# Optimization experiments

Measured on AMD Instinct MI355X. Metric: run time of the kernel, lower is better.

Reference implementation:

```python
import jax, jax.numpy as jnp
import numpy as np

ROPE_THETA = 10000.0

def _apply_rope(t):
    # t: [B, H, S, D]; rotate interleaved even/odd pairs
    B, H, S, D = t.shape
    inv_freq = 1.0 / (ROPE_THETA ** (jnp.arange(0, D, 2, dtype=jnp.float32) / D))  # [D/2]
    ang = jnp.arange(S, dtype=jnp.float32)[:, None] * inv_freq[None, :]            # [S, D/2]
    cos = jnp.cos(ang)[None, None]  # [1,1,S,D/2]
    sin = jnp.sin(ang)[None, None]
    te = t[..., 0::2]
    to = t[..., 1::2]
    re = te * cos - to * sin
    ro = te * sin + to * cos
    out = jnp.stack([re, ro], axis=-1).reshape(B, H, S, D)
    return out

def setup_inputs() -> dict:
    key = jax.random.key(0)
    ks = jax.random.split(key, 5)
    B, S, DIM = 2, 2048, 2048
    x = jax.random.normal(ks[0], (B, S, DIM), dtype=jnp.float32)
    scale = 0.02
    Wq = jax.random.normal(ks[1], (DIM, DIM), dtype=jnp.float32) * scale
    Wk = jax.random.normal(ks[2], (DIM, DIM), dtype=jnp.float32) * scale
    Wv = jax.random.normal(ks[3], (DIM, DIM), dtype=jnp.float32) * scale
    Wo = jax.random.normal(ks[4], (DIM, DIM), dtype=jnp.float32) * scale
    return {"x": x, "Wq": Wq, "Wk": Wk, "Wv": Wv, "Wo": Wo}

def reference(x, Wq, Wk, Wv, Wo):
    B, S, DIM = x.shape
    H = 16
    HD = DIM // H
    # nn.Linear(bias=False) with weight [out,in]: y = x @ W.T; here W stored [in,out]
    q = (x @ Wq).reshape(B, S, H, HD).transpose(0, 2, 1, 3)  # [B,H,S,HD]
    k = (x @ Wk).reshape(B, S, H, HD).transpose(0, 2, 1, 3)
    v = (x @ Wv).reshape(B, S, H, HD).transpose(0, 2, 1, 3)
    q = _apply_rope(q)
    k = _apply_rope(k)
    scores = jnp.einsum('bhqd,bhkd->bhqk', q, k) / jnp.sqrt(jnp.float32(HD))  # [B,H,S,S]
    causal = jnp.tril(jnp.ones((S, S), dtype=bool))
    scores = jnp.where(causal[None, None], scores, jnp.float32(-jnp.inf))
    attn = jax.nn.softmax(scores, axis=-1)
    out = jnp.einsum('bhqk,bhkd->bhqd', attn, v)            # [B,H,S,HD]
    out = out.transpose(0, 2, 1, 3).reshape(B, S, DIM)
    return out @ Wo  # output projection (dropout is identity in eval)
```

## Files before the change

### kernel.cpp

```cpp
#include <hip/hip_runtime.h>
#include <hip/hip_bf16.h>
#include <math.h>

typedef __bf16 bf16;
typedef __attribute__((ext_vector_type(2))) __bf16 bf16x2;
typedef __attribute__((ext_vector_type(4))) __bf16 bf16x4;
typedef __attribute__((ext_vector_type(8))) __bf16 bf16x8;
typedef __attribute__((ext_vector_type(4))) float f32x4;

#define LDS_ASYNC16(gptr, lptr)                                                        \
  __builtin_amdgcn_global_load_lds(                                                    \
      (const __attribute__((address_space(1))) void*)(gptr),                           \
      (__attribute__((address_space(3))) void*)(lptr), 16, 0, 0)

constexpr int BATCH = 2, SEQ = 2048, DIM = 2048, NH = 16, HD = 128;
constexpr float QSC = 0.12751744f;
constexpr float FREQC = 0.20762050593046f;

template <int CTRL>
__device__ __forceinline__ float dpp_mov_f(float x) {
  return __int_as_float(__builtin_amdgcn_update_dpp(
      __float_as_int(x), __float_as_int(x), CTRL, 0xf, 0xf, false));
}
__device__ __forceinline__ float rowmax16(float x) {
  x = fmaxf(x, dpp_mov_f<0x121>(x));
  x = fmaxf(x, dpp_mov_f<0x122>(x));
  x = fmaxf(x, dpp_mov_f<0x124>(x));
  x = fmaxf(x, dpp_mov_f<0x128>(x));
  return x;
}
__device__ __forceinline__ float rowsum16(float x) {
  x += dpp_mov_f<0x121>(x);
  x += dpp_mov_f<0x122>(x);
  x += dpp_mov_f<0x124>(x);
  x += dpp_mov_f<0x128>(x);
  return x;
}

__global__ void cvt_f32_to_bf16(const float4* __restrict__ in,
                                bf16x4* __restrict__ out, int n4) {
  int i = blockIdx.x * blockDim.x + threadIdx.x;
  if (i >= n4) return;
  float4 v = in[i];
  bf16x4 o;
  o[0] = (bf16)v.x; o[1] = (bf16)v.y; o[2] = (bf16)v.z; o[3] = (bf16)v.w;
  out[i] = o;
}

__global__ void transpose_w4(const float* __restrict__ W0, const float* __restrict__ W1,
                             const float* __restrict__ W2, const float* __restrict__ W3,
                             bf16* __restrict__ T0, bf16* __restrict__ T3) {
  __shared__ float tile[32][33];
  const int z = blockIdx.z;
  const float* W = (z == 0) ? W0 : (z == 1) ? W1 : (z == 2) ? W2 : W3;
  bf16* WT = (z == 3) ? T3 : (T0 + (size_t)z * DIM * DIM);
  int tx = threadIdx.x, ty = threadIdx.y;
  int bx = blockIdx.x * 32, by = blockIdx.y * 32;
#pragma unroll
  for (int j = 0; j < 32; j += 8)
    tile[ty + j][tx] = W[(size_t)(by + ty + j) * DIM + bx + tx];
  __syncthreads();
#pragma unroll
  for (int j = 0; j < 32; j += 8)
    WT[(size_t)(bx + ty + j) * DIM + by + tx] = (bf16)tile[tx][ty + j];
}


__global__ __launch_bounds__(256) void gemm_qkv(const bf16* __restrict__ A,
                                                const bf16* __restrict__ BT,
                                                bf16* __restrict__ Qb,
                                                bf16* __restrict__ Kb,
                                                bf16* __restrict__ VTo) {
  __shared__ __attribute__((aligned(16))) bf16 As[128 * 64];
  __shared__ __attribute__((aligned(16))) bf16 Bs[128 * 64];
  const int tid = threadIdx.x;
  const int w = tid >> 6, lane = tid & 63;
  const int quad = lane >> 4, ln = lane & 15;
  const int m0 = blockIdx.y * 128, n0 = blockIdx.x * 128;
  const int wm = (w >> 1) * 64, wn = (w & 1) * 64;
  const int l7 = ln & 7;
  f32x4 acc[4][4] = {};

  for (int k0 = 0; k0 < DIM; k0 += 64) {
#pragma unroll
    for (int i = 0; i < 4; ++i) {
      const int c = i * 256 + tid;
      const int row = c >> 3, p = c & 7;
      LDS_ASYNC16(A  + (size_t)(m0 + row) * DIM + k0 + ((p ^ (row & 7)) * 8),
                  As + (size_t)(i * 256 + w * 64) * 8);
      LDS_ASYNC16(BT + (size_t)(n0 + row) * DIM + k0 + ((p ^ (row & 7)) * 8),
                  Bs + (size_t)(i * 256 + w * 64) * 8);
    }
    __syncthreads();
#pragma unroll
    for (int kh = 0; kh < 2; ++kh) {
      bf16x8 af[4], bfr[4];
#pragma unroll
      for (int t = 0; t < 4; ++t)
        af[t] = *(const bf16x8*)(As + (wm + t * 16 + ln) * 64 +
                                 (((kh * 4 + quad) ^ l7) * 8));
#pragma unroll
      for (int t = 0; t < 4; ++t)
        bfr[t] = *(const bf16x8*)(Bs + (wn + t * 16 + ln) * 64 +
                                  (((kh * 4 + quad) ^ l7) * 8));
#pragma unroll
      for (int mt = 0; mt < 4; ++mt)
#pragma unroll
        for (int nt = 0; nt < 4; ++nt)
          acc[mt][nt] = __builtin_amdgcn_mfma_f32_16x16x32_bf16(
              af[mt], bfr[nt], acc[mt][nt], 0, 0, 0);
    }
    __syncthreads();
  }

  const int sel = n0 >> 11;
  if (sel == 2) {
#pragma unroll
    for (int mt = 0; mt < 4; ++mt)
#pragma unroll
      for (int nt = 0; nt < 4; ++nt) {
        int gr = m0 + wm + mt * 16 + quad * 4;
        int fc = (n0 + wn + nt * 16 + ln) & 2047;
        int b = gr >> 11, s0 = gr & (SEQ - 1);
        int h = fc >> 7, d = fc & (HD - 1);
        bf16x4 pk;
#pragma unroll
        for (int r = 0; r < 4; ++r) pk[r] = (bf16)acc[mt][nt][r];
        *(bf16x4*)(VTo + ((size_t)((b * NH + h) * HD + d)) * SEQ + s0) = pk;
      }
  } else {
    bf16* Dst = sel ? Kb : Qb;
    const float osc = sel ? 1.0f : QSC;
#pragma unroll
    for (int nt = 0; nt < 4; ++nt) {
      int gc = n0 + wn + nt * 16 + ln;
      int fc = gc & 2047, d = fc & (HD - 1);
      float freq = exp2f(-(float)(d >> 1) * FREQC);
      bool ev = !(d & 1);
#pragma unroll
      for (int mt = 0; mt < 4; ++mt) {
#pragma unroll
        for (int r = 0; r < 4; ++r) {
          int gr = m0 + wm + mt * 16 + quad * 4 + r;
          int s = gr & (SEQ - 1);
          float ang = (float)s * freq;
          float sn, cs;
          __sincosf(ang, &sn, &cs);
          float own = acc[mt][nt][r];
          float oth = __shfl_xor(own, 1);
          float res = ev ? (own * cs - oth * sn) : (oth * sn + own * cs);
          Dst[(size_t)gr * DIM + fc] = (bf16)(res * osc);
        }
      }
    }
  }
}

template <int MODE>
__global__ __launch_bounds__(256) void gemm_bt(const bf16* __restrict__ A,
                                               const bf16* __restrict__ BT,
                                               void* __restrict__ C) {
  __shared__ __attribute__((aligned(16))) bf16 As[128 * 64];
  __shared__ __attribute__((aligned(16))) bf16 Bs[128 * 64];
  const int tid = threadIdx.x;
  const int w = tid >> 6, lane = tid & 63;
  const int quad = lane >> 4, ln = lane & 15;
  const int m0 = blockIdx.y * 128, n0 = blockIdx.x * 128;
  const int wm = (w >> 1) * 64, wn = (w & 1) * 64;
  const int l7 = ln & 7;
  f32x4 acc[4][4] = {};

  for (int k0 = 0; k0 < DIM; k0 += 64) {
#pragma unroll
    for (int i = 0; i < 4; ++i) {
      const int c = i * 256 + tid;
      const int row = c >> 3, p = c & 7;
      LDS_ASYNC16(A  + (size_t)(m0 + row) * DIM + k0 + ((p ^ (row & 7)) * 8),
                  As + (size_t)(i * 256 + w * 64) * 8);
      LDS_ASYNC16(BT + (size_t)(n0 + row) * DIM + k0 + ((p ^ (row & 7)) * 8),
                  Bs + (size_t)(i * 256 + w * 64) * 8);
    }
    __syncthreads();
#pragma unroll
    for (int kh = 0; kh < 2; ++kh) {
      bf16x8 af[4], bfr[4];
#pragma unroll
      for (int t = 0; t < 4; ++t)
        af[t] = *(const bf16x8*)(As + (wm + t * 16 + ln) * 64 +
                                 (((kh * 4 + quad) ^ l7) * 8));
#pragma unroll
      for (int t = 0; t < 4; ++t)
        bfr[t] = *(const bf16x8*)(Bs + (wn + t * 16 + ln) * 64 +
                                  (((kh * 4 + quad) ^ l7) * 8));
#pragma unroll
      for (int mt = 0; mt < 4; ++mt)
#pragma unroll
        for (int nt = 0; nt < 4; ++nt)
          acc[mt][nt] = __builtin_amdgcn_mfma_f32_16x16x32_bf16(
              af[mt], bfr[nt], acc[mt][nt], 0, 0, 0);
    }
    __syncthreads();
  }

  if (MODE == 0) {
    bf16* Co = (bf16*)C;
#pragma unroll
    for (int mt = 0; mt < 4; ++mt)
#pragma unroll
      for (int nt = 0; nt < 4; ++nt) {
        int gr = m0 + wm + mt * 16 + quad * 4;
        int gc = n0 + wn + nt * 16 + ln;
#pragma unroll
        for (int r = 0; r < 4; ++r)
          Co[(size_t)(gr + r) * DIM + gc] = (bf16)acc[mt][nt][r];
      }
  } else {
    float* Co = (float*)C;
#pragma unroll
    for (int mt = 0; mt < 4; ++mt)
#pragma unroll
      for (int nt = 0; nt < 4; ++nt) {
        int gr = m0 + wm + mt * 16 + quad * 4;
        int gc = n0 + wn + nt * 16 + ln;
#pragma unroll
        for (int r = 0; r < 4; ++r)
          Co[(size_t)(gr + r) * DIM + gc] = acc[mt][nt][r];
      }
  }
}

__device__ __forceinline__ int ml_off(int t) {
  return (t < 10) ? 2 * (t - 5) : (t < 15) ? 10 + 3 * (t - 10) : 25;
}
__device__ __forceinline__ int op_off(int t) {
  return (t < 10) ? (t - 5) : (t < 15) ? 5 + 2 * (t - 10) : 15;
}

constexpr int PSTR = 72;
__global__ __launch_bounds__(256) void flash_attn(
    const bf16* __restrict__ Q, const bf16* __restrict__ K,
    const bf16* __restrict__ VT, bf16* __restrict__ O,
    bf16* __restrict__ Opart, float* __restrict__ Mpart,
    float* __restrict__ Lpart) {
  __shared__ __attribute__((aligned(16))) bf16 Ks[64 * 128];
  __shared__ __attribute__((aligned(16))) bf16 VTs[128 * 64];
  __shared__ __attribute__((aligned(16))) bf16 Ps[4][32 * PSTR];
  const int tid = threadIdx.x;
  const int w = tid >> 6, lane = tid & 63, quad = lane >> 4, ln = lane & 15;
  const int lb = blockIdx.x;
  const int low3 = lb & 7, rest = lb >> 3;
  const int e = rest % 34;
  const int bh = (rest / 34) * 8 + low3;
  int t, c0, nc;
  if (e < 5)       { t = e;                  c0 = 0;               nc = 1; }
  else if (e < 15) { t = 5 + ((e - 5) >> 1); c0 = (e - 5) & 1;     nc = 2; }
  else if (e < 30) { int q = (e - 15) / 3;   t = 10 + q; c0 = (e - 15) - 3 * q; nc = 3; }
  else             { t = 15;                 c0 = e - 30;          nc = 4; }
  const int q0 = t * 128;
  const int ktN = 2 * (t + 1);
  const int kt0 = c0 * 10;
  const int kt1 = min(kt0 + 10, ktN);
  const bool chunked = (nc > 1);
  const int b = bh >> 4, h = bh & 15;

  bf16x8 qf[2][4];
#pragma unroll
  for (int mt = 0; mt < 2; ++mt)
#pragma unroll
    for (int kc = 0; kc < 4; ++kc)
      qf[mt][kc] = *(const bf16x8*)(Q + ((size_t)b * SEQ + q0 + w * 32 + mt * 16 + ln) * DIM +
                                    h * HD + kc * 32 + quad * 8);
  f32x4 o[2][8] = {};
  float mst[2][4], lst[2][4];
#pragma unroll
  for (int mt = 0; mt < 2; ++mt)
#pragma unroll
    for (int r = 0; r < 4; ++r) { mst[mt][r] = -1e30f; lst[mt][r] = 0.f; }

  for (int kt = kt0; kt < kt1; ++kt) {
    __syncthreads();
#pragma unroll
    for (int i = 0; i < 4; ++i) {
      const int c = i * 256 + tid;
      LDS_ASYNC16(K + ((size_t)b * SEQ + kt * 64 + (c >> 4)) * DIM + h * HD +
                      (((c & 15) ^ ((c >> 4) & 15)) * 8),
                  Ks + (size_t)(i * 256 + w * 64) * 8);
      LDS_ASYNC16(VT + ((size_t)((b * NH + h) * HD) + (c >> 3)) * SEQ + kt * 64 +
                      (((c & 7) ^ ((c >> 3) & 7)) * 8),
                  VTs + (size_t)(i * 256 + w * 64) * 8);
    }
    __syncthreads();

    f32x4 s[2][4] = {};
#pragma unroll
    for (int nt = 0; nt < 4; ++nt) {
      bf16x8 kf[4];
#pragma unroll
      for (int kc = 0; kc < 4; ++kc)
        kf[kc] = *(const bf16x8*)(Ks + (nt * 16 + ln) * 128 +
                                  (((kc * 4 + quad) ^ ln) * 8));
#pragma unroll
      for (int kc = 0; kc < 4; ++kc)
#pragma unroll
        for (int mt = 0; mt < 2; ++mt)
          s[mt][nt] = __builtin_amdgcn_mfma_f32_16x16x32_bf16(
              qf[mt][kc], kf[kc], s[mt][nt], 0, 0, 0);
    }

    const bool diag = (kt * 64 + 63 > q0);
    if (diag) {
#pragma unroll
      for (int mt = 0; mt < 2; ++mt)
#pragma unroll
        for (int nt = 0; nt < 4; ++nt)
#pragma unroll
          for (int r = 0; r < 4; ++r) {
            int kg = kt * 64 + nt * 16 + ln;
            int qg = q0 + w * 32 + mt * 16 + quad * 4 + r;
            if (kg > qg) s[mt][nt][r] = -1e30f;
          }
    }

#pragma unroll
    for (int mt = 0; mt < 2; ++mt)
#pragma unroll
      for (int r = 0; r < 4; ++r) {
        float rm = fmaxf(fmaxf(s[mt][0][r], s[mt][1][r]),
                         fmaxf(s[mt][2][r], s[mt][3][r]));
        rm = rowmax16(rm);
        float mold = mst[mt][r];
        float mnew = fmaxf(mold, rm);
        float alpha = exp2f(mold - mnew);
        mst[mt][r] = mnew;
        float rs = 0.f;
#pragma unroll
        for (int nt = 0; nt < 4; ++nt) {
          float p = exp2f(s[mt][nt][r] - mnew);
          rs += p;
          Ps[w][(mt * 16 + quad * 4 + r) * PSTR + nt * 16 + ln] = (bf16)p;
        }
        lst[mt][r] = lst[mt][r] * alpha + rs;
#pragma unroll
        for (int nd = 0; nd < 8; ++nd) o[mt][nd][r] *= alpha;
      }
    __syncthreads();

#pragma unroll
    for (int kc2 = 0; kc2 < 2; ++kc2) {
      bf16x8 pf[2];
#pragma unroll
      for (int mt = 0; mt < 2; ++mt)
        pf[mt] = *(const bf16x8*)(&Ps[w][(mt * 16 + ln) * PSTR + kc2 * 32 + quad * 8]);
#pragma unroll
      for (int nd = 0; nd < 8; ++nd) {
        bf16x8 vf = *(const bf16x8*)(VTs + (nd * 16 + ln) * 64 +
                                     (((kc2 * 4 + quad) ^ (ln & 7)) * 8));
#pragma unroll
        for (int mt = 0; mt < 2; ++mt)
          o[mt][nd] = __builtin_amdgcn_mfma_f32_16x16x32_bf16(
              pf[mt], vf, o[mt][nd], 0, 0, 0);
      }
    }
  }

  if (!chunked) {
#pragma unroll
    for (int mt = 0; mt < 2; ++mt)
#pragma unroll
      for (int r = 0; r < 4; ++r) {
        float inv = 1.f / rowsum16(lst[mt][r]);
        int qg = q0 + w * 32 + mt * 16 + quad * 4 + r;
#pragma unroll
        for (int nd = 0; nd < 8; ++nd)
          O[((size_t)b * SEQ + qg) * DIM + h * HD + nd * 16 + ln] =
              (bf16)(o[mt][nd][r] * inv);
      }
  } else {
    const int mls = bh * 29 + ml_off(t) + c0;
    bf16* Op = (c0 == 0) ? nullptr
                         : Opart + (size_t)(bh * 18 + op_off(t) + (c0 - 1)) * (128 * 128);
#pragma unroll
    for (int mt = 0; mt < 2; ++mt)
#pragma unroll
      for (int r = 0; r < 4; ++r) {
        float l = rowsum16(lst[mt][r]);
        int qr = w * 32 + mt * 16 + quad * 4 + r;
        if (ln == 0) {
          Mpart[mls * 128 + qr] = mst[mt][r];
          Lpart[mls * 128 + qr] = l;
        }
        if (c0 == 0) {
#pragma unroll
          for (int nd = 0; nd < 8; ++nd)
            O[((size_t)b * SEQ + q0 + qr) * DIM + h * HD + nd * 16 + ln] =
                (bf16)o[mt][nd][r];
        } else {
#pragma unroll
          for (int nd = 0; nd < 8; ++nd)
            Op[qr * 128 + nd * 16 + ln] = (bf16)o[mt][nd][r];
        }
      }
  }
}

__global__ __launch_bounds__(256) void flash_merge(const bf16* __restrict__ Opart,
                                                   const float* __restrict__ Mpart,
                                                   const float* __restrict__ Lpart,
                                                   bf16* __restrict__ O) {
  const int bh = blockIdx.x;
  const int t = 5 + blockIdx.y;
  const int nc = (t < 10) ? 2 : (t < 15) ? 3 : 4;
  const int b = bh >> 4, h = bh & 15;
  const int row = threadIdx.x >> 1, half = threadIdx.x & 1;
  const int mlb = bh * 29 + ml_off(t);
  float m[4], l[4], wt[4];
  float M = -1e30f;
  for (int c = 0; c < nc; ++c) {
    m[c] = Mpart[(mlb + c) * 128 + row];
    l[c] = Lpart[(mlb + c) * 128 + row];
    M = fmaxf(M, m[c]);
  }
  float wsum = 0.f;
  for (int c = 0; c < nc; ++c) { wt[c] = exp2f(m[c] - M); wsum += wt[c] * l[c]; }
  const float inv = 1.f / wsum;
  bf16* dst = O + ((size_t)b * SEQ + t * 128 + row) * DIM + h * HD + half * 64;
  const bf16* pb = Opart + (size_t)(bh * 18 + op_off(t)) * (128 * 128) + row * 128 + half * 64;
#pragma unroll
  for (int j = 0; j < 8; ++j) {
    bf16x8 a0 = *(const bf16x8*)(dst + j * 8);
    float acc[8];
#pragma unroll
    for (int k = 0; k < 8; ++k) acc[k] = wt[0] * (float)a0[k];
    for (int c = 1; c < nc; ++c) {
      bf16x8 a = *(const bf16x8*)(pb + (size_t)(c - 1) * (128 * 128) + j * 8);
#pragma unroll
      for (int k = 0; k < 8; ++k) acc[k] += wt[c] * (float)a[k];
    }
    bf16x8 o8;
#pragma unroll
    for (int k = 0; k < 8; ++k) o8[k] = (bf16)(acc[k] * inv);
    *(bf16x8*)(dst + j * 8) = o8;
  }
}

extern "C" void kernel_launch(void* const* d_in, const int* in_sizes, int n_in,
                              void* d_out, int out_size, void* d_ws, size_t ws_size,
                              hipStream_t stream) {
  (void)in_sizes; (void)n_in; (void)out_size; (void)ws_size;
  const float* x  = (const float*)d_in[0];
  const float* Wq = (const float*)d_in[1];
  const float* Wk = (const float*)d_in[2];
  const float* Wv = (const float*)d_in[3];
  const float* Wo = (const float*)d_in[4];

  char* ws = (char*)d_ws;
  const size_t MB = 1u << 20;
  const size_t WB = (size_t)DIM * DIM * 2;
  bf16* WTqkv = (bf16*)(ws);
  bf16* WoT   = (bf16*)(ws + 3 * WB);
  bf16* xb    = (bf16*)(ws + 32 * MB);
  bf16* Qb    = (bf16*)(ws + 48 * MB);
  bf16* Kb    = (bf16*)(ws + 64 * MB);
  bf16* VT    = (bf16*)(ws + 80 * MB);
  bf16* Ab    = xb;
  bf16*  Opart = (bf16*)(ws);
  float* Mpart = (float*)(ws + 19 * MB);
  float* Lpart = (float*)(ws + 19 * MB + 512 * 1024);

  int n4 = BATCH * SEQ * DIM / 4;
  cvt_f32_to_bf16<<<n4 / 256, 256, 0, stream>>>((const float4*)x, (bf16x4*)xb, n4);
  dim3 tb(32, 8), tg(DIM / 32, DIM / 32, 4);
  transpose_w4<<<tg, tb, 0, stream>>>(Wq, Wk, Wv, Wo, WTqkv, WoT);

  dim3 qg(3 * DIM / 128, BATCH * SEQ / 128);
  gemm_qkv<<<qg, 256, 0, stream>>>(xb, WTqkv, Qb, Kb, VT);

  flash_attn<<<34 * BATCH * NH, 256, 0, stream>>>(Qb, Kb, VT, Ab, Opart, Mpart, Lpart);
  dim3 mg(BATCH * NH, 11);
  flash_merge<<<mg, 256, 0, stream>>>(Opart, Mpart, Lpart, Ab);

  dim3 gg(DIM / 128, BATCH * SEQ / 128);
  gemm_bt<2><<<gg, 256, 0, stream>>>(Ab, WoT, d_out);
}
```

Before: 444.5 us.

## Rewrite QKV GEMM as 256x256 tile with multi-buffered async LDS pipeline

The fused QKV projection GEMM moves from a 128x128 tile with 4 waves and a single LDS buffer to a 256x256 tile with 8 waves. It now double-buffers K-slices in LDS, issuing async global-to-LDS loads for future slices while MFMAs run on the current one, and uses s_setprio around the MFMA bursts. A remapped 1D grid with block-id swizzling is added for L2 locality. The aim is to hide global-load latency and raise arithmetic intensity, at the cost of more registers per thread, more LDS and fewer workgroups (384).

```diff
diff --git a/kernel.cpp b/kernel.cpp
--- a/kernel.cpp
+++ b/kernel.cpp
@@ -65,88 +65,171 @@
     WT[(size_t)(bx + ty + j) * DIM + by + tx] = (bf16)tile[tx][ty + j];
 }
 
-
-__global__ __launch_bounds__(256) void gemm_qkv(const bf16* __restrict__ A,
+__device__ __forceinline__ void stage_half(const bf16* __restrict__ src, int g0, int ks,
+                                           bf16* lds, int w, int lane) {
+#pragma unroll
+  for (int j = 0; j < 2; ++j) {
+    const int u = (j * 8 + w) * 64 + lane;
+    const int row = u >> 2;
+    const int kc = (u & 3) ^ ((u >> 3) & 3);
+    LDS_ASYNC16(src + (size_t)(g0 + row) * DIM + ks + kc * 8,
+                lds + (size_t)((j * 8 + w) * 64) * 8);
+  }
+}
+
+__global__ __launch_bounds__(512) void gemm_qkv(const bf16* __restrict__ A,
                                                 const bf16* __restrict__ BT,
                                                 bf16* __restrict__ Qb,
                                                 bf16* __restrict__ Kb,
                                                 bf16* __restrict__ VTo) {
-  __shared__ __attribute__((aligned(16))) bf16 As[128 * 64];
-  __shared__ __attribute__((aligned(16))) bf16 Bs[128 * 64];
+  constexpr int RSZ = 256 * 32;
+  constexpr int NT = DIM / 64;
+  __shared__ __attribute__((aligned(16))) bf16 As[4 * RSZ];
+  __shared__ __attribute__((aligned(16))) bf16 Bs[4 * RSZ];
   const int tid = threadIdx.x;
   const int w = tid >> 6, lane = tid & 63;
   const int quad = lane >> 4, ln = lane & 15;
-  const int m0 = blockIdx.y * 128, n0 = blockIdx.x * 128;
-  const int wm = (w >> 1) * 64, wn = (w & 1) * 64;
-  const int l7 = ln & 7;
-  f32x4 acc[4][4] = {};
-
-  for (int k0 = 0; k0 < DIM; k0 += 64) {
-#pragma unroll
-    for (int i = 0; i < 4; ++i) {
-      const int c = i * 256 + tid;
-      const int row = c >> 3, p = c & 7;
-      LDS_ASYNC16(A  + (size_t)(m0 + row) * DIM + k0 + ((p ^ (row & 7)) * 8),
-                  As + (size_t)(i * 256 + w * 64) * 8);
-      LDS_ASYNC16(BT + (size_t)(n0 + row) * DIM + k0 + ((p ^ (row & 7)) * 8),
-                  Bs + (size_t)(i * 256 + w * 64) * 8);
-    }
-    __syncthreads();
-#pragma unroll
-    for (int kh = 0; kh < 2; ++kh) {
-      bf16x8 af[4], bfr[4];
-#pragma unroll
-      for (int t = 0; t < 4; ++t)
-        af[t] = *(const bf16x8*)(As + (wm + t * 16 + ln) * 64 +
-                                 (((kh * 4 + quad) ^ l7) * 8));
-#pragma unroll
-      for (int t = 0; t < 4; ++t)
-        bfr[t] = *(const bf16x8*)(Bs + (wn + t * 16 + ln) * 64 +
-                                  (((kh * 4 + quad) ^ l7) * 8));
-#pragma unroll
-      for (int mt = 0; mt < 4; ++mt)
-#pragma unroll
-        for (int nt = 0; nt < 4; ++nt)
-          acc[mt][nt] = __builtin_amdgcn_mfma_f32_16x16x32_bf16(
-              af[mt], bfr[nt], acc[mt][nt], 0, 0, 0);
-    }
-    __syncthreads();
+  const int wm = w >> 2, wn = w & 3;
+  const int lb = blockIdx.x;
+  const int wgid = (lb & 7) * 48 + (lb >> 3);
+  const int bx = wgid % 24, by = wgid / 24;
+  const int m0 = by * 256, n0 = bx * 256;
+  const int pc = (quad ^ ((ln >> 1) & 3)) * 8;
+  const int aoff = wm * 128 + ln;
+  const int boff = wn * 64 + ln;
+
+  f32x4 acc[8][4] = {};
+
+  stage_half(A,  m0, 0,  As + 0 * RSZ, w, lane);
+  stage_half(BT, n0, 0,  Bs + 0 * RSZ, w, lane);
+  stage_half(A,  m0, 32, As + 1 * RSZ, w, lane);
+  stage_half(BT, n0, 32, Bs + 1 * RSZ, w, lane);
+  stage_half(A,  m0, 64, As + 2 * RSZ, w, lane);
+  stage_half(BT, n0, 64, Bs + 2 * RSZ, w, lane);
+  stage_half(BT, n0, 96, Bs + 3 * RSZ, w, lane);
+  asm volatile("s_waitcnt vmcnt(6)" ::: "memory");
+  __builtin_amdgcn_s_barrier();
+
+#pragma unroll 2
+  for (int t = 0; t < NT; ++t) {
+    const int b2 = (t & 1) * 2;
+    const bf16* Ab0 = As + b2 * RSZ;
+    const bf16* Ab1 = Ab0 + RSZ;
+    const bf16* Bb0 = Bs + b2 * RSZ;
+    const bf16* Bb1 = Bb0 + RSZ;
+    bf16x8 af[4], bfr[4];
+
+#pragma unroll
+    for (int i = 0; i < 4; ++i)
+      af[i] = *(const bf16x8*)(Ab0 + (aoff + i * 16) * 32 + pc);
+#pragma unroll
+    for (int i = 0; i < 4; ++i)
+      bfr[i] = *(const bf16x8*)(Bb0 + (boff + i * 16) * 32 + pc);
+    if (t + 1 < NT)
+      stage_half(A, m0, (t + 1) * 64 + 32, As + ((((t + 1) & 1) * 2) + 1) * RSZ, w, lane);
+    __builtin_amdgcn_s_barrier();
+    asm volatile("s_waitcnt lgkmcnt(0)" ::: "memory");
+    __builtin_amdgcn_s_setprio(1);
+#pragma unroll
+    for (int mf = 0; mf < 4; ++mf)
+#pragma unroll
+      for (int nf = 0; nf < 4; ++nf)
+        acc[mf][nf] = __builtin_amdgcn_mfma_f32_16x16x32_bf16(
+            af[mf], bfr[nf], acc[mf][nf], 0, 0, 0);
+    __builtin_amdgcn_s_setprio(0);
+    __builtin_amdgcn_s_barrier();
+
+#pragma unroll
+    for (int i = 0; i < 4; ++i)
+      af[i] = *(const bf16x8*)(Ab0 + (aoff + 64 + i * 16) * 32 + pc);
+    if (t + 2 < NT)
+      stage_half(BT, n0, (t + 2) * 64, Bs + b2 * RSZ, w, lane);
+    __builtin_amdgcn_s_barrier();
+    asm volatile("s_waitcnt lgkmcnt(0)" ::: "memory");
+    __builtin_amdgcn_s_setprio(1);
+#pragma unroll
+    for (int mf = 0; mf < 4; ++mf)
+#pragma unroll
+      for (int nf = 0; nf < 4; ++nf)
+        acc[4 + mf][nf] = __builtin_amdgcn_mfma_f32_16x16x32_bf16(
+            af[mf], bfr[nf], acc[4 + mf][nf], 0, 0, 0);
+    __builtin_amdgcn_s_setprio(0);
+    __builtin_amdgcn_s_barrier();
+
+#pragma unroll
+    for (int i = 0; i < 4; ++i)
+      af[i] = *(const bf16x8*)(Ab1 + (aoff + i * 16) * 32 + pc);
+#pragma unroll
+    for (int i = 0; i < 4; ++i)
+      bfr[i] = *(const bf16x8*)(Bb1 + (boff + i * 16) * 32 + pc);
+    if (t + 2 < NT)
+      stage_half(A, m0, (t + 2) * 64, As + b2 * RSZ, w, lane);
+    __builtin_amdgcn_s_barrier();
+    asm volatile("s_waitcnt lgkmcnt(0)" ::: "memory");
+    __builtin_amdgcn_s_setprio(1);
+#pragma unroll
+    for (int mf = 0; mf < 4; ++mf)
+#pragma unroll
+      for (int nf = 0; nf < 4; ++nf)
+        acc[mf][nf] = __builtin_amdgcn_mfma_f32_16x16x32_bf16(
+            af[mf], bfr[nf], acc[mf][nf], 0, 0, 0);
+    __builtin_amdgcn_s_setprio(0);
+    __builtin_amdgcn_s_barrier();
+
+#pragma unroll
+    for (int i = 0; i < 4; ++i)
+      af[i] = *(const bf16x8*)(Ab1 + (aoff + 64 + i * 16) * 32 + pc);
+    if (t + 2 < NT)
+      stage_half(BT, n0, (t + 2) * 64 + 32, Bs + (b2 + 1) * RSZ, w, lane);
+    __builtin_amdgcn_s_barrier();
+    asm volatile("s_waitcnt lgkmcnt(0)" ::: "memory");
+    __builtin_amdgcn_s_setprio(1);
+#pragma unroll
+    for (int mf = 0; mf < 4; ++mf)
+#pragma unroll
+      for (int nf = 0; nf < 4; ++nf)
+        acc[4 + mf][nf] = __builtin_amdgcn_mfma_f32_16x16x32_bf16(
+            af[mf], bfr[nf], acc[4 + mf][nf], 0, 0, 0);
+    __builtin_amdgcn_s_setprio(0);
+    if (t + 2 < NT) asm volatile("s_waitcnt vmcnt(6)" ::: "memory");
+    else            asm volatile("s_waitcnt vmcnt(0)" ::: "memory");
+    __builtin_amdgcn_s_barrier();
   }
 
   const int sel = n0 >> 11;
   if (sel == 2) {
 #pragma unroll
-    for (int mt = 0; mt < 4; ++mt)
-#pragma unroll
-      for (int nt = 0; nt < 4; ++nt) {
-        int gr = m0 + wm + mt * 16 + quad * 4;
-        int fc = (n0 + wn + nt * 16 + ln) & 2047;
-        int b = gr >> 11, s0 = gr & (SEQ - 1);
+    for (int mf = 0; mf < 8; ++mf)
+#pragma unroll
+      for (int nf = 0; nf < 4; ++nf) {
+        int gr = m0 + wm * 128 + mf * 16 + quad * 4;
+        int fc = (n0 + wn * 64 + nf * 16 + ln) & 2047;
+        int bb = gr >> 11, s0 = gr & (SEQ - 1);
         int h = fc >> 7, d = fc & (HD - 1);
         bf16x4 pk;
 #pragma unroll
-        for (int r = 0; r < 4; ++r) pk[r] = (bf16)acc[mt][nt][r];
-        *(bf16x4*)(VTo + ((size_t)((b * NH + h) * HD + d)) * SEQ + s0) = pk;
+        for (int r = 0; r < 4; ++r) pk[r] = (bf16)acc[mf][nf][r];
+        *(bf16x4*)(VTo + ((size_t)((bb * NH + h) * HD + d)) * SEQ + s0) = pk;
       }
   } else {
     bf16* Dst = sel ? Kb : Qb;
     const float osc = sel ? 1.0f : QSC;
 #pragma unroll
-    for (int nt = 0; nt < 4; ++nt) {
-      int gc = n0 + wn + nt * 16 + ln;
+    for (int nf = 0; nf < 4; ++nf) {
+      int gc = n0 + wn * 64 + nf * 16 + ln;
       int fc = gc & 2047, d = fc & (HD - 1);
       float freq = exp2f(-(float)(d >> 1) * FREQC);
       bool ev = !(d & 1);
 #pragma unroll
-      for (int mt = 0; mt < 4; ++mt) {
+      for (int mf = 0; mf < 8; ++mf) {
 #pragma unroll
         for (int r = 0; r < 4; ++r) {
-          int gr = m0 + wm + mt * 16 + quad * 4 + r;
+          int gr = m0 + wm * 128 + mf * 16 + quad * 4 + r;
           int s = gr & (SEQ - 1);
           float ang = (float)s * freq;
           float sn, cs;
           __sincosf(ang, &sn, &cs);
-          float own = acc[mt][nt][r];
+          float own = acc[mf][nf][r];
           float oth = __shfl_xor(own, 1);
           float res = ev ? (own * cs - oth * sn) : (oth * sn + own * cs);
           Dst[(size_t)gr * DIM + fc] = (bf16)(res * osc);
@@ -472,8 +555,7 @@
   dim3 tb(32, 8), tg(DIM / 32, DIM / 32, 4);
   transpose_w4<<<tg, tb, 0, stream>>>(Wq, Wk, Wv, Wo, WTqkv, WoT);
 
-  dim3 qg(3 * DIM / 128, BATCH * SEQ / 128);
-  gemm_qkv<<<qg, 256, 0, stream>>>(xb, WTqkv, Qb, Kb, VT);
+  gemm_qkv<<<24 * 16, 512, 0, stream>>>(xb, WTqkv, Qb, Kb, VT);
 
   flash_attn<<<34 * BATCH * NH, 256, 0, stream>>>(Qb, Kb, VT, Ab, Opart, Mpart, Lpart);
   dim3 mg(BATCH * NH, 11);
```

Result: slower. 458.3 us (+3.1%).
